# Performance work log

Hardware: AMD Instinct MI355X
Metric: run time of the kernel (lower is better)

The kernel has to match this reference:

```python
import jax, jax.numpy as jnp
import numpy as np

H = W = 56; C = 128; WS = 7; SS = 3; NH = 4; P = 5
HD = C // NH
NWH = H // WS; NWW = W // WS; NW = NWH * NWW
NTOK = WS * WS          # 49 spatial tokens per window
N = NTOK + P            # 54 tokens per window incl. prompts
MLP_H = 4 * C


def _rel_pos_index():
    coords = np.stack(np.meshgrid(np.arange(WS), np.arange(WS), indexing='ij'))  # (2,ws,ws)
    cf = coords.reshape(2, -1)
    rel = (cf[:, :, None] - cf[:, None, :]).transpose(1, 2, 0).copy()
    rel[:, :, 0] += WS - 1
    rel[:, :, 1] += WS - 1
    rel[:, :, 0] *= 2 * WS - 1
    return rel.sum(-1)  # (49,49) int


def _attn_mask():
    # standard shifted-window mask, -100 on cross-region pairs, padded with 0 for prompts
    img = np.zeros((H, W))
    cnt = 0
    for hs in (slice(0, -WS), slice(-WS, -SS), slice(-SS, None)):
        for ws_ in (slice(0, -WS), slice(-WS, -SS), slice(-SS, None)):
            img[hs, ws_] = cnt
            cnt += 1
    mw = img.reshape(NWH, WS, NWW, WS).transpose(0, 2, 1, 3).reshape(-1, NTOK)
    am = mw[:, None, :] - mw[:, :, None]
    am = np.where(am != 0, -100.0, 0.0).astype(np.float32)  # (nW,49,49)
    return np.pad(am, ((0, 0), (P, 0), (P, 0)))  # (nW,54,54)


def layer_norm(x, g, b):
    mu = x.mean(-1, keepdims=True)
    var = ((x - mu) ** 2).mean(-1, keepdims=True)
    return (x - mu) * jax.lax.rsqrt(var + 1e-5) * g + b


def setup_inputs() -> dict:
    key = jax.random.key(0)
    ks = jax.random.split(key, 8)
    s = 0.02
    return {
        'x': jax.random.normal(ks[0], (64, P + H * W, C), jnp.float32),
        'norm1_g': jnp.ones((C,), jnp.float32),
        'norm1_b': jnp.zeros((C,), jnp.float32),
        'qkv_w': jax.random.normal(ks[1], (C, 3 * C), jnp.float32) * s,
        'qkv_b': jnp.zeros((3 * C,), jnp.float32),
        'proj_w': jax.random.normal(ks[2], (C, C), jnp.float32) * s,
        'proj_b': jnp.zeros((C,), jnp.float32),
        'rpb_table': jax.random.normal(ks[3], ((2 * WS - 1) ** 2, NH), jnp.float32) * s,
        'norm2_g': jnp.ones((C,), jnp.float32),
        'norm2_b': jnp.zeros((C,), jnp.float32),
        'fc1_w': jax.random.normal(ks[4], (C, MLP_H), jnp.float32) * s,
        'fc1_b': jnp.zeros((MLP_H,), jnp.float32),
        'fc2_w': jax.random.normal(ks[5], (MLP_H, C), jnp.float32) * s,
        'fc2_b': jnp.zeros((C,), jnp.float32),
    }


def reference(x, norm1_g, norm1_b, qkv_w, qkv_b, proj_w, proj_b, rpb_table,
              norm2_g, norm2_b, fc1_w, fc1_b, fc2_w, fc2_b):
    B = x.shape[0]
    shortcut = x
    xn = layer_norm(x, norm1_g, norm1_b)
    prompt = xn[:, :P]                                  # (B,P,C)
    xs = xn[:, P:].reshape(B, H, W, C)
    xs = jnp.roll(xs, (-SS, -SS), axis=(1, 2))          # cyclic shift
    # window partition -> (B*nW, 49, C), batch-major
    xw = xs.reshape(B, NWH, WS, NWW, WS, C).transpose(0, 1, 3, 2, 4, 5).reshape(B * NW, NTOK, C)
    # prompt expansion: VPT uses expand(nW,...).reshape(-1) => window-major ordering (faithful)
    pe = jnp.broadcast_to(prompt[None], (NW, B, P, C)).reshape(NW * B, P, C)
    xw = jnp.concatenate([pe, xw], axis=1)              # (B*nW, N, C)
    # windowed multi-head attention
    qkv = (xw @ qkv_w + qkv_b).reshape(-1, N, 3, NH, HD).transpose(2, 0, 3, 1, 4)
    q, k, v = qkv[0] * (HD ** -0.5), qkv[1], qkv[2]     # (B*nW, NH, N, HD)
    attn = jnp.einsum('whnd,whmd->whnm', q, k)
    rpb = rpb_table[jnp.asarray(_rel_pos_index().reshape(-1))].reshape(NTOK, NTOK, NH).transpose(2, 0, 1)
    rpb = jnp.pad(rpb, ((0, 0), (P, 0), (P, 0)))        # zeros for prompt rows/cols
    attn = attn + rpb[None]
    mask = jnp.asarray(_attn_mask())                    # (nW,N,N)
    attn = attn.reshape(B, NW, NH, N, N) + mask[None, :, None]
    attn = jax.nn.softmax(attn.reshape(-1, NH, N, N), axis=-1)
    out = jnp.einsum('whnm,whmd->whnd', attn, v).transpose(0, 2, 1, 3).reshape(-1, N, C)
    out = out @ proj_w + proj_b
    # split prompts back out, average across windows (view(-1,B,...) => window-major, faithful)
    prompt_out = out[:, :P].reshape(NW, B, P, C).mean(0)
    spat = out[:, P:].reshape(B, NWH, NWW, WS, WS, C).transpose(0, 1, 3, 2, 4, 5).reshape(B, H, W, C)
    spat = jnp.roll(spat, (SS, SS), axis=(1, 2)).reshape(B, H * W, C)
    xo = jnp.concatenate([prompt_out, spat], axis=1)
    x = shortcut + xo
    h = layer_norm(x, norm2_g, norm2_b)
    h = jax.nn.gelu(h @ fc1_w + fc1_b, approximate=False)
    h = h @ fc2_w + fc2_b
    return x + h
```

## Files before the change

### kernel.cpp

```cpp
#include <hip/hip_runtime.h>
#include <hip/hip_bf16.h>
#include <math.h>


typedef __attribute__((ext_vector_type(8))) short bf16x8;
typedef __attribute__((ext_vector_type(4))) float f32x4;
typedef __attribute__((ext_vector_type(4))) unsigned short u16x4;

__device__ __forceinline__ float bf2f(unsigned short u) {
  union { unsigned int i; float f; } v; v.i = ((unsigned)u) << 16; return v.f;
}
__device__ __forceinline__ unsigned short f2b(float f) {
  __hip_bfloat16 b = __float2bfloat16(f);
  return *reinterpret_cast<unsigned short*>(&b);
}

__global__ __launch_bounds__(256) void convert_wt(const float* __restrict__ w,
    __hip_bfloat16* __restrict__ wt, int K, int N)
{
  int idx = blockIdx.x * 256 + threadIdx.x;
  if (idx >= N * K) return;
  int n = idx / K, k = idx % K;
  wt[idx] = __float2bfloat16(w[(size_t)k * N + n]);
}

__global__ __launch_bounds__(256) void bias_gen(const float* __restrict__ rpb,
    __hip_bfloat16* __restrict__ tab)
{
  int w = blockIdx.x >> 2, h = blockIdx.x & 3;
  int wh = w >> 3, ww = w & 7;
  #pragma unroll
  for (int e = 0; e < 16; ++e) {
    int fi = e * 256 + threadIdx.x;
    int q = fi >> 6, k = fi & 63;
    float v;
    if (k >= 54) {
      v = -INFINITY;
    } else {
      v = 0.f;
      if (q >= 5 && q < 54 && k >= 5) {
        int tq = q - 5, tk = k - 5;
        int aq = tq / 7, bq_ = tq % 7, ak = tk / 7, bk = tk % 7;
        int dh = aq - ak + 6, dw = bq_ - bk + 6;
        v = rpb[(dh * 13 + dw) * 4 + h];
        int rq = wh * 7 + aq, cq = ww * 7 + bq_;
        int rk = wh * 7 + ak, ck = ww * 7 + bk;
        int zq = (rq < 49 ? 0 : (rq < 53 ? 1 : 2)) * 3 + (cq < 49 ? 0 : (cq < 53 ? 1 : 2));
        int zk = (rk < 49 ? 0 : (rk < 53 ? 1 : 2)) * 3 + (ck < 49 ? 0 : (ck < 53 ? 1 : 2));
        if (zq != zk) v += -100.f;
      }
      v *= 1.44269504088896f;
    }
    tab[((size_t)blockIdx.x << 12) + fi] = __float2bfloat16(v);
  }
}

__global__ __launch_bounds__(256, 3) void phase1_fused(
    const float* __restrict__ x,
    const float* __restrict__ n1g, const float* __restrict__ n1b,
    const __hip_bfloat16* __restrict__ w_qkv, const float* __restrict__ qkv_b,
    const __hip_bfloat16* __restrict__ w_prj, const float* __restrict__ proj_b,
    const __hip_bfloat16* __restrict__ bias_tab,
    float* __restrict__ out, float* __restrict__ pbuf)
{
  __shared__ short lds[24576];
  short* xn = lds;
  const int tid = threadIdx.x;
  const int wv = tid >> 6, lane = tid & 63;
  const int c = lane & 15, g = lane >> 4;
  const int gi = blockIdx.x;
  const int w = gi & 63;
  short* Lh = lds + wv * 6144;

  float v0a[14], v1a[14];
  #pragma unroll
  for (int rr = 0; rr < 14; ++rr) {
    int row = wv + rr * 4;
    int rowc = (row < 54) ? row : 0;
    int src;
    if (rowc < 5) {
      src = (gi & 63) * 3141 + rowc;
    } else {
      int b = gi >> 6, t = rowc - 5;
      int hp = (w >> 3) * 7 + t / 7 + 3; if (hp >= 56) hp -= 56;
      int wp = (w & 7) * 7 + t % 7 + 3;  if (wp >= 56) wp -= 56;
      src = b * 3141 + 5 + hp * 56 + wp;
    }
    const float* xr = x + (size_t)src * 128;
    v0a[rr] = xr[lane];
    v1a[rr] = xr[lane + 64];
  }
  #pragma unroll
  for (int rr = 0; rr < 14; ++rr) {
    int row = wv + rr * 4;
    if (row < 54) {
      float v0 = v0a[rr], v1 = v1a[rr];
      float s = v0 + v1, s2 = v0 * v0 + v1 * v1;
      #pragma unroll
      for (int off = 32; off > 0; off >>= 1) {
        s  += __shfl_xor(s,  off);
        s2 += __shfl_xor(s2, off);
      }
      float mu = s * (1.f / 128.f);
      float var = s2 * (1.f / 128.f) - mu * mu;
      float rs = rsqrtf(var + 1e-5f);
      float y0 = (v0 - mu) * rs * n1g[lane]      + n1b[lane];
      float y1 = (v1 - mu) * rs * n1g[lane + 64] + n1b[lane + 64];
      int f = (row & 15) >> 1;
      int ca = lane, cb = lane + 64;
      xn[row * 128 + (((ca >> 3) ^ f) << 3) + (ca & 7)] = (short)f2b(y0);
      xn[row * 128 + (((cb >> 3) ^ f) << 3) + (cb & 7)] = (short)f2b(y1);
    }
  }
  for (int idx = tid; idx < 1280; idx += 256) xn[54 * 128 + idx] = 0;
  __syncthreads();

  bf16x8 af[4][4];
  #pragma unroll
  for (int ks = 0; ks < 4; ++ks)
    #pragma unroll
    for (int mi = 0; mi < 4; ++mi) {
      int row = mi * 16 + c;
      af[ks][mi] = *(const bf16x8*)(xn + row * 128 +
                    (((ks * 4 + g) ^ ((row & 15) >> 1)) << 3));
    }
  const unsigned short* bt = (const unsigned short*)bias_tab + ((size_t)(w * 4 + wv) << 12);
  u16x4 bb[4][4];
  #pragma unroll
  for (int ni = 0; ni < 4; ++ni)
    #pragma unroll
    for (int mi = 0; mi < 4; ++mi)
      bb[ni][mi] = *(const u16x4*)(bt + (ni * 16 + c) * 64 + mi * 16 + g * 4);
  __syncthreads();

  {
    #pragma unroll
    for (int t = 0; t < 6; ++t) {
      int m = t >> 1;
      int chb = (t & 1) * 16;
      int n0 = m * 128 + wv * 32 + chb;
      bf16x8 bfr[4];
      #pragma unroll
      for (int ks = 0; ks < 4; ++ks)
        bfr[ks] = *(const bf16x8*)(w_qkv + (size_t)(n0 + c) * 128 + ks * 32 + g * 8);
      f32x4 acct[4] = {};
      __builtin_amdgcn_s_setprio(1);
      #pragma unroll
      for (int ks = 0; ks < 4; ++ks)
        #pragma unroll
        for (int mi = 0; mi < 4; ++mi)
          acct[mi] = __builtin_amdgcn_mfma_f32_16x16x32_bf16(
              bfr[ks], af[ks][mi], acct[mi], 0, 0, 0);
      __builtin_amdgcn_s_setprio(0);
      f32x4 bq4 = *(const f32x4*)(qkv_b + n0 + g * 4);
      int cpart = (chb >> 3) + (g >> 1);
      #pragma unroll
      for (int mi = 0; mi < 4; ++mi) {
        int tok = mi * 16 + c;
        int swz = (m == 2) ? ((tok >> 3) & 3) : ((tok >> 1) & 3);
        u16x4 pw;
        #pragma unroll
        for (int r = 0; r < 4; ++r) pw[r] = f2b(acct[mi][r] + bq4[r]);
        *(u16x4*)(Lh + m * 2048 + tok * 32 + ((cpart ^ swz) << 3) + (g & 1) * 4) = pw;
      }
    }
  }

  {
    const int h = wv;
    bf16x8 kf[4], bq[4];
    #pragma unroll
    for (int mi = 0; mi < 4; ++mi) {
      int tok = mi * 16 + c;
      kf[mi] = *(const bf16x8*)(Lh + 2048 + tok * 32 + ((g ^ ((tok >> 1) & 3)) << 3));
    }
    #pragma unroll
    for (int ni = 0; ni < 4; ++ni) {
      int q = ni * 16 + c;
      bq[ni] = *(const bf16x8*)(Lh + q * 32 + ((g ^ ((q >> 1) & 3)) << 3));
    }
    f32x4 acc[4][4] = {};
    __builtin_amdgcn_s_setprio(1);
    #pragma unroll
    for (int mi = 0; mi < 4; ++mi)
      #pragma unroll
      for (int ni = 0; ni < 4; ++ni)
        acc[mi][ni] = __builtin_amdgcn_mfma_f32_16x16x32_bf16(kf[mi], bq[ni], acc[mi][ni], 0, 0, 0);
    __builtin_amdgcn_s_setprio(0);

    const float SC = 0.17677669529663689f * 1.44269504088896f;
    #pragma unroll
    for (int ni = 0; ni < 4; ++ni)
      #pragma unroll
      for (int mi = 0; mi < 4; ++mi)
        #pragma unroll
        for (int r = 0; r < 4; ++r)
          acc[mi][ni][r] = acc[mi][ni][r] * SC + bf2f(bb[ni][mi][r]);

    #pragma unroll
    for (int ni = 0; ni < 4; ++ni) {
      float m2 = -3.0e38f;
      #pragma unroll
      for (int mi = 0; mi < 4; ++mi)
        #pragma unroll
        for (int r = 0; r < 4; ++r)
          m2 = fmaxf(m2, acc[mi][ni][r]);
      m2 = fmaxf(m2, __shfl_xor(m2, 16, 64));
      m2 = fmaxf(m2, __shfl_xor(m2, 32, 64));
      float sm = 0.f;
      #pragma unroll
      for (int mi = 0; mi < 4; ++mi)
        #pragma unroll
        for (int r = 0; r < 4; ++r) {
          float p = exp2f(acc[mi][ni][r] - m2);
          acc[mi][ni][r] = p;
          sm += p;
        }
      sm += __shfl_xor(sm, 16, 64);
      sm += __shfl_xor(sm, 32, 64);
      float inv = 1.0f / sm;
      int q = ni * 16 + c;
      #pragma unroll
      for (int mi = 0; mi < 4; ++mi) {
        u16x4 pw;
        #pragma unroll
        for (int r = 0; r < 4; ++r) pw[r] = f2b(acc[mi][ni][r] * inv);
        int chp = (mi * 2 + (g >> 1)) ^ (q & 7);
        *(u16x4*)(Lh + q * 64 + chp * 8 + (g & 1) * 4) = pw;
      }
    }

    f32x4 acc2[2][4] = {};
    #pragma unroll
    for (int ks = 0; ks < 2; ++ks) {
      bf16x8 pa[4];
      #pragma unroll
      for (int qi = 0; qi < 4; ++qi) {
        int q = qi * 16 + c;
        int chk = (ks * 4 + g) ^ (q & 7);
        pa[qi] = *(const bf16x8*)(Lh + q * 64 + chk * 8);
      }
      bf16x8 vb[2];
      #pragma unroll
      for (int di = 0; di < 2; ++di) {
        #pragma unroll
        for (int j = 0; j < 8; ++j) {
          int k = ks * 32 + g * 8 + j;
          int chv = ((di * 2 + (c >> 3)) ^ g);
          vb[di][j] = Lh[4096 + k * 32 + chv * 8 + (c & 7)];
        }
      }
      __builtin_amdgcn_s_setprio(1);
      #pragma unroll
      for (int qi = 0; qi < 4; ++qi)
        #pragma unroll
        for (int di = 0; di < 2; ++di)
          acc2[di][qi] = __builtin_amdgcn_mfma_f32_16x16x32_bf16(vb[di], pa[qi], acc2[di][qi], 0, 0, 0);
      __builtin_amdgcn_s_setprio(0);
    }

    __syncthreads();
    #pragma unroll
    for (int di = 0; di < 2; ++di) {
      int chunk = h * 4 + di * 2 + (g >> 1);
      #pragma unroll
      for (int qi = 0; qi < 4; ++qi) {
        int tok = qi * 16 + c;
        u16x4 pw;
        #pragma unroll
        for (int r = 0; r < 4; ++r) pw[r] = f2b(acc2[di][qi][r]);
        *(u16x4*)(xn + tok * 128 + ((chunk ^ (c >> 1)) << 3) + (g & 1) * 4) = pw;
      }
    }
  }
  __syncthreads();

  {
    f32x4 accp[4][2] = {};
    #pragma unroll
    for (int ks = 0; ks < 4; ++ks) {
      bf16x8 afp[4];
      #pragma unroll
      for (int mi = 0; mi < 4; ++mi) {
        int row = mi * 16 + c;
        afp[mi] = *(const bf16x8*)(xn + row * 128 +
                   (((ks * 4 + g) ^ ((row & 15) >> 1)) << 3));
      }
      bf16x8 wfp[2];
      #pragma unroll
      for (int ni = 0; ni < 2; ++ni)
        wfp[ni] = *(const bf16x8*)(w_prj +
            (size_t)(wv * 32 + ni * 16 + c) * 128 + ks * 32 + g * 8);
      #pragma unroll
      for (int mi = 0; mi < 4; ++mi)
        #pragma unroll
        for (int ni = 0; ni < 2; ++ni)
          accp[mi][ni] = __builtin_amdgcn_mfma_f32_16x16x32_bf16(
              afp[mi], wfp[ni], accp[mi][ni], 0, 0, 0);
    }
    float pb[2];
    pb[0] = proj_b[wv * 32 + c];
    pb[1] = proj_b[wv * 32 + 16 + c];
    #pragma unroll
    for (int mi = 0; mi < 4; ++mi) {
      #pragma unroll
      for (int r = 0; r < 4; ++r) {
        int tok = mi * 16 + g * 4 + r;
        if (tok < 54) {
          if (tok < 5) {
            #pragma unroll
            for (int ni = 0; ni < 2; ++ni) {
              int gcol = wv * 32 + ni * 16 + c;
              pbuf[((size_t)gi * 5 + tok) * 128 + gcol] = accp[mi][ni][r] + pb[ni];
            }
          } else {
            int b = gi >> 6, tt = tok - 5;
            int rr2 = (w >> 3) * 7 + tt / 7 + 3; if (rr2 >= 56) rr2 -= 56;
            int cc = (w & 7) * 7 + tt % 7 + 3;   if (cc >= 56) cc -= 56;
            size_t ob = ((size_t)b * 3141 + 5 + rr2 * 56 + cc) * 128;
            #pragma unroll
            for (int ni = 0; ni < 2; ++ni) {
              int gcol = wv * 32 + ni * 16 + c;
              out[ob + gcol] = x[ob + gcol] + accp[mi][ni][r] + pb[ni];
            }
          }
        }
      }
    }
  }
}

__global__ __launch_bounds__(128) void prompt_reduce(const float* __restrict__ x,
    const float* __restrict__ pbuf, float* __restrict__ out)
{
  int bp = blockIdx.x;
  int b = bp / 5, p = bp % 5;
  int c = threadIdx.x;
  float s = 0.f;
  for (int w = 0; w < 64; ++w)
    s += pbuf[((size_t)(w * 64 + b) * 5 + p) * 128 + c];
  size_t oidx = ((size_t)b * 3141 + p) * 128 + c;
  out[oidx] = x[oidx] + s * (1.f / 64.f);
}

__device__ __forceinline__ void mlp_fc1(const short* __restrict__ xn,
    short* __restrict__ dst, const __hip_bfloat16* __restrict__ w1t,
    const float* __restrict__ b1, int s, int wv, int c, int g)
{
  bf16x8 wf[4][2];
  #pragma unroll
  for (int ks = 0; ks < 4; ++ks)
    #pragma unroll
    for (int ni = 0; ni < 2; ++ni)
      wf[ks][ni] = *(const bf16x8*)(w1t +
          (size_t)(s * 128 + wv * 32 + ni * 16 + c) * 128 + ks * 32 + g * 8);
  f32x4 acc1[2][4] = {};
  #pragma unroll
  for (int ks = 0; ks < 4; ++ks) {
    bf16x8 af[4];
    #pragma unroll
    for (int mi = 0; mi < 4; ++mi) {
      int row = mi * 16 + c;
      af[mi] = *(const bf16x8*)(xn + row * 128 +
                                (((ks * 4 + g) ^ ((row & 15) >> 1)) << 3));
    }
    #pragma unroll
    for (int mi = 0; mi < 4; ++mi)
      #pragma unroll
      for (int ni = 0; ni < 2; ++ni)
        acc1[ni][mi] = __builtin_amdgcn_mfma_f32_16x16x32_bf16(
            wf[ks][ni], af[mi], acc1[ni][mi], 0, 0, 0);
  }
  #pragma unroll
  for (int ni = 0; ni < 2; ++ni) {
    f32x4 b1v = *(const f32x4*)(b1 + s * 128 + wv * 32 + ni * 16 + g * 4);
    int chunk = wv * 4 + ni * 2 + (g >> 1);
    #pragma unroll
    for (int mi = 0; mi < 4; ++mi) {
      int tok = mi * 16 + c;
      u16x4 pw;
      #pragma unroll
      for (int r = 0; r < 4; ++r) {
        float t = acc1[ni][mi][r] + b1v[r];
        float u = t * (0.7978845608028654f + 0.0356774081f * t * t);
        float e = exp2f(-2.8853900817779268f * u);
        t = t * __builtin_amdgcn_rcpf(1.0f + e);
        pw[r] = f2b(t);
      }
      *(u16x4*)(dst + tok * 128 + ((chunk ^ (c >> 1)) << 3) + (g & 1) * 4) = pw;
    }
  }
}

__device__ __forceinline__ void mlp_fc2(const short* __restrict__ hsrc,
    const __hip_bfloat16* __restrict__ w2t, f32x4 (&acc2)[4][2],
    int s, int wv, int c, int g)
{
  bf16x8 wf[4][2];
  #pragma unroll
  for (int ks = 0; ks < 4; ++ks)
    #pragma unroll
    for (int ni = 0; ni < 2; ++ni)
      wf[ks][ni] = *(const bf16x8*)(w2t +
          (size_t)(wv * 32 + ni * 16 + c) * 512 + s * 128 + ks * 32 + g * 8);
  #pragma unroll
  for (int ks = 0; ks < 4; ++ks) {
    bf16x8 af[4];
    #pragma unroll
    for (int mi = 0; mi < 4; ++mi) {
      int row = mi * 16 + c;
      af[mi] = *(const bf16x8*)(hsrc + row * 128 +
                                (((ks * 4 + g) ^ ((row & 15) >> 1)) << 3));
    }
    #pragma unroll
    for (int mi = 0; mi < 4; ++mi)
      #pragma unroll
      for (int ni = 0; ni < 2; ++ni)
        acc2[mi][ni] = __builtin_amdgcn_mfma_f32_16x16x32_bf16(
            af[mi], wf[ks][ni], acc2[mi][ni], 0, 0, 0);
  }
}

__global__ __launch_bounds__(256, 3) void mlp_fused(
    const float* __restrict__ xin,
    const float* __restrict__ gamma, const float* __restrict__ beta,
    const __hip_bfloat16* __restrict__ w1t, const float* __restrict__ b1,
    const __hip_bfloat16* __restrict__ w2t, const float* __restrict__ b2,
    float* __restrict__ outp)
{
  __shared__ short xn[8192];
  __shared__ short hb[2][8192];
  const int tid = threadIdx.x;
  const int wv = tid >> 6, lane = tid & 63;
  const int c = lane & 15, g = lane >> 4;
  const int r0 = blockIdx.x * 64;

  float v0a[16], v1a[16];
  #pragma unroll
  for (int rr = 0; rr < 16; ++rr) {
    int row = wv * 16 + rr;
    const float* xr = xin + (size_t)(r0 + row) * 128;
    v0a[rr] = xr[lane];
    v1a[rr] = xr[lane + 64];
  }
  #pragma unroll
  for (int rr = 0; rr < 16; ++rr) {
    int row = wv * 16 + rr;
    float v0 = v0a[rr], v1 = v1a[rr];
    float s = v0 + v1, s2 = v0 * v0 + v1 * v1;
    #pragma unroll
    for (int off = 32; off > 0; off >>= 1) {
      s  += __shfl_xor(s,  off);
      s2 += __shfl_xor(s2, off);
    }
    float mu = s * (1.f / 128.f);
    float var = s2 * (1.f / 128.f) - mu * mu;
    float rs = rsqrtf(var + 1e-5f);
    float y0 = (v0 - mu) * rs * gamma[lane]      + beta[lane];
    float y1 = (v1 - mu) * rs * gamma[lane + 64] + beta[lane + 64];
    int f = (row & 15) >> 1;
    int ca = lane, cb = lane + 64;
    xn[row * 128 + (((ca >> 3) ^ f) << 3) + (ca & 7)] = (short)f2b(y0);
    xn[row * 128 + (((cb >> 3) ^ f) << 3) + (cb & 7)] = (short)f2b(y1);
  }
  __syncthreads();

  mlp_fc1(xn, hb[0], w1t, b1, 0, wv, c, g);
  __syncthreads();

  f32x4 acc2[4][2] = {};
  #pragma unroll
  for (int s = 0; s < 4; ++s) {
    if (s < 3) mlp_fc1(xn, hb[(s + 1) & 1], w1t, b1, s + 1, wv, c, g);
    mlp_fc2(hb[s & 1], w2t, acc2, s, wv, c, g);
    if (s < 3) __syncthreads();
  }

  #pragma unroll
  for (int mi = 0; mi < 4; ++mi) {
    #pragma unroll
    for (int r = 0; r < 4; ++r) {
      int row = r0 + mi * 16 + g * 4 + r;
      #pragma unroll
      for (int ni = 0; ni < 2; ++ni) {
        int col = wv * 32 + ni * 16 + c;
        size_t o = (size_t)row * 128 + col;
        outp[o] = acc2[mi][ni][r] + b2[col] + xin[o];
      }
    }
  }
}

extern "C" void kernel_launch(void* const* d_in, const int* in_sizes, int n_in,
                              void* d_out, int out_size, void* d_ws, size_t ws_size,
                              hipStream_t stream) {
  const float* x      = (const float*)d_in[0];
  const float* n1g    = (const float*)d_in[1];
  const float* n1b    = (const float*)d_in[2];
  const float* qkv_w  = (const float*)d_in[3];
  const float* qkv_b  = (const float*)d_in[4];
  const float* proj_w = (const float*)d_in[5];
  const float* proj_b = (const float*)d_in[6];
  const float* rpb    = (const float*)d_in[7];
  const float* n2g    = (const float*)d_in[8];
  const float* n2b    = (const float*)d_in[9];
  const float* fc1w   = (const float*)d_in[10];
  const float* fc1b   = (const float*)d_in[11];
  const float* fc2w   = (const float*)d_in[12];
  const float* fc2b   = (const float*)d_in[13];
  float* out = (float*)d_out;
  char* ws = (char*)d_ws;

  __hip_bfloat16* wbuf = (__hip_bfloat16*)ws;
  __hip_bfloat16* w_qkv = wbuf;
  __hip_bfloat16* w_prj = wbuf + 49152;
  __hip_bfloat16* w_fc1 = wbuf + 65536;
  __hip_bfloat16* w_fc2 = wbuf + 131072;
  __hip_bfloat16* bias_tab = (__hip_bfloat16*)(ws + 393216);
  float* pbuf = (float*)(ws + 2490368);

  hipLaunchKernelGGL(convert_wt, dim3(192), dim3(256), 0, stream, qkv_w, w_qkv, 128, 384);
  hipLaunchKernelGGL(convert_wt, dim3(64),  dim3(256), 0, stream, proj_w, w_prj, 128, 128);
  hipLaunchKernelGGL(convert_wt, dim3(256), dim3(256), 0, stream, fc1w,  w_fc1, 128, 512);
  hipLaunchKernelGGL(convert_wt, dim3(256), dim3(256), 0, stream, fc2w,  w_fc2, 512, 128);
  hipLaunchKernelGGL(bias_gen, dim3(256), dim3(256), 0, stream, rpb, bias_tab);

  hipLaunchKernelGGL(phase1_fused, dim3(4096), dim3(256), 0, stream,
                     x, n1g, n1b, w_qkv, qkv_b, w_prj, proj_b, bias_tab, out, pbuf);
  hipLaunchKernelGGL(prompt_reduce, dim3(320), dim3(128), 0, stream, x, pbuf, out);

  hipLaunchKernelGGL(mlp_fused, dim3(3141), dim3(256), 0, stream,
                     out, n2g, n2b, w_fc1, fc1b, w_fc2, fc2b, out);
  (void)in_sizes; (void)n_in; (void)out_size; (void)ws_size;
}
```

Baseline: 323.8 us.

## Keep Q/K and softmax probabilities in registers, shrink LDS for higher occupancy

Q and K projections are computed with a permuted weight-row order so their MFMA accumulators can be packed directly into B/A fragments for the QK^T MFMA, skipping the LDS round trip. Softmax probabilities are likewise packed in registers as operands for the PV MFMA, and only V is staged in LDS (per-wave 2048 shorts). This cuts LDS from 48KB to 32KB, lets launch bounds rise to 4 blocks per CU, and removes one barrier. The cost is higher register pressure under the tighter bound, which may cause spills; the rel-pos bias load is also moved later.

```diff
diff --git a/kernel.cpp b/kernel.cpp
--- a/kernel.cpp
+++ b/kernel.cpp
@@ -14,6 +14,10 @@
   __hip_bfloat16 b = __float2bfloat16(f);
   return *reinterpret_cast<unsigned short*>(&b);
 }
+__device__ __forceinline__ unsigned pkbf(float lo, float hi) {
+  return ((unsigned)f2b(hi) << 16) | (unsigned)f2b(lo);
+}
+union Pk8 { bf16x8 v; unsigned w[4]; };
 
 __global__ __launch_bounds__(256) void convert_wt(const float* __restrict__ w,
     __hip_bfloat16* __restrict__ wt, int K, int N)
@@ -55,7 +59,7 @@
   }
 }
 
-__global__ __launch_bounds__(256, 3) void phase1_fused(
+__global__ __launch_bounds__(256, 4) void phase1_fused(
     const float* __restrict__ x,
     const float* __restrict__ n1g, const float* __restrict__ n1b,
     const __hip_bfloat16* __restrict__ w_qkv, const float* __restrict__ qkv_b,
@@ -63,15 +67,17 @@
     const __hip_bfloat16* __restrict__ bias_tab,
     float* __restrict__ out, float* __restrict__ pbuf)
 {
-  __shared__ short lds[24576];
+  __shared__ short lds[16384];
   short* xn = lds;
   const int tid = threadIdx.x;
   const int wv = tid >> 6, lane = tid & 63;
   const int c = lane & 15, g = lane >> 4;
   const int gi = blockIdx.x;
   const int w = gi & 63;
-  short* Lh = lds + wv * 6144;
-
+  short* Vb = lds + 8192 + wv * 2048;
+
+  float g0 = n1g[lane], g1 = n1g[lane + 64];
+  float b0 = n1b[lane], b1 = n1b[lane + 64];
   float v0a[14], v1a[14];
   #pragma unroll
   for (int rr = 0; rr < 14; ++rr) {
@@ -104,8 +110,8 @@
       float mu = s * (1.f / 128.f);
       float var = s2 * (1.f / 128.f) - mu * mu;
       float rs = rsqrtf(var + 1e-5f);
-      float y0 = (v0 - mu) * rs * n1g[lane]      + n1b[lane];
-      float y1 = (v1 - mu) * rs * n1g[lane + 64] + n1b[lane + 64];
+      float y0 = (v0 - mu) * rs * g0 + b0;
+      float y1 = (v1 - mu) * rs * g1 + b1;
       int f = (row & 15) >> 1;
       int ca = lane, cb = lane + 64;
       xn[row * 128 + (((ca >> 3) ^ f) << 3) + (ca & 7)] = (short)f2b(y0);
@@ -124,25 +130,19 @@
       af[ks][mi] = *(const bf16x8*)(xn + row * 128 +
                     (((ks * 4 + g) ^ ((row & 15) >> 1)) << 3));
     }
-  const unsigned short* bt = (const unsigned short*)bias_tab + ((size_t)(w * 4 + wv) << 12);
-  u16x4 bb[4][4];
-  #pragma unroll
-  for (int ni = 0; ni < 4; ++ni)
-    #pragma unroll
-    for (int mi = 0; mi < 4; ++mi)
-      bb[ni][mi] = *(const u16x4*)(bt + (ni * 16 + c) * 64 + mi * 16 + g * 4);
-  __syncthreads();
-
-  {
-    #pragma unroll
-    for (int t = 0; t < 6; ++t) {
-      int m = t >> 1;
-      int chb = (t & 1) * 16;
-      int n0 = m * 128 + wv * 32 + chb;
+
+  bf16x8 bq[4], kf[4];
+  #pragma unroll
+  for (int qk = 0; qk < 2; ++qk) {
+    f32x4 a0[4] = {}, a1[4] = {};
+    #pragma unroll
+    for (int tt = 0; tt < 2; ++tt) {
       bf16x8 bfr[4];
       #pragma unroll
       for (int ks = 0; ks < 4; ++ks)
-        bfr[ks] = *(const bf16x8*)(w_qkv + (size_t)(n0 + c) * 128 + ks * 32 + g * 8);
+        bfr[ks] = *(const bf16x8*)(w_qkv +
+            (size_t)(qk * 128 + wv * 32 + (c >> 2) * 8 + tt * 4 + (c & 3)) * 128 +
+            ks * 32 + g * 8);
       f32x4 acct[4] = {};
       __builtin_amdgcn_s_setprio(1);
       #pragma unroll
@@ -152,125 +152,156 @@
           acct[mi] = __builtin_amdgcn_mfma_f32_16x16x32_bf16(
               bfr[ks], af[ks][mi], acct[mi], 0, 0, 0);
       __builtin_amdgcn_s_setprio(0);
-      f32x4 bq4 = *(const f32x4*)(qkv_b + n0 + g * 4);
-      int cpart = (chb >> 3) + (g >> 1);
-      #pragma unroll
-      for (int mi = 0; mi < 4; ++mi) {
-        int tok = mi * 16 + c;
-        int swz = (m == 2) ? ((tok >> 3) & 3) : ((tok >> 1) & 3);
-        u16x4 pw;
-        #pragma unroll
-        for (int r = 0; r < 4; ++r) pw[r] = f2b(acct[mi][r] + bq4[r]);
-        *(u16x4*)(Lh + m * 2048 + tok * 32 + ((cpart ^ swz) << 3) + (g & 1) * 4) = pw;
-      }
-    }
-  }
-
-  {
-    const int h = wv;
-    bf16x8 kf[4], bq[4];
-    #pragma unroll
-    for (int mi = 0; mi < 4; ++mi) {
-      int tok = mi * 16 + c;
-      kf[mi] = *(const bf16x8*)(Lh + 2048 + tok * 32 + ((g ^ ((tok >> 1) & 3)) << 3));
-    }
-    #pragma unroll
-    for (int ni = 0; ni < 4; ++ni) {
-      int q = ni * 16 + c;
-      bq[ni] = *(const bf16x8*)(Lh + q * 32 + ((g ^ ((q >> 1) & 3)) << 3));
-    }
-    f32x4 acc[4][4] = {};
-    __builtin_amdgcn_s_setprio(1);
-    #pragma unroll
-    for (int mi = 0; mi < 4; ++mi)
-      #pragma unroll
-      for (int ni = 0; ni < 4; ++ni)
-        acc[mi][ni] = __builtin_amdgcn_mfma_f32_16x16x32_bf16(kf[mi], bq[ni], acc[mi][ni], 0, 0, 0);
-    __builtin_amdgcn_s_setprio(0);
-
-    const float SC = 0.17677669529663689f * 1.44269504088896f;
-    #pragma unroll
-    for (int ni = 0; ni < 4; ++ni)
-      #pragma unroll
-      for (int mi = 0; mi < 4; ++mi)
-        #pragma unroll
-        for (int r = 0; r < 4; ++r)
-          acc[mi][ni][r] = acc[mi][ni][r] * SC + bf2f(bb[ni][mi][r]);
-
-    #pragma unroll
-    for (int ni = 0; ni < 4; ++ni) {
-      float m2 = -3.0e38f;
-      #pragma unroll
-      for (int mi = 0; mi < 4; ++mi)
-        #pragma unroll
-        for (int r = 0; r < 4; ++r)
-          m2 = fmaxf(m2, acc[mi][ni][r]);
-      m2 = fmaxf(m2, __shfl_xor(m2, 16, 64));
-      m2 = fmaxf(m2, __shfl_xor(m2, 32, 64));
-      float sm = 0.f;
+      f32x4 bv = *(const f32x4*)(qkv_b + qk * 128 + wv * 32 + g * 8 + tt * 4);
       #pragma unroll
       for (int mi = 0; mi < 4; ++mi)
         #pragma unroll
         for (int r = 0; r < 4; ++r) {
-          float p = exp2f(acc[mi][ni][r] - m2);
-          acc[mi][ni][r] = p;
-          sm += p;
+          float t = acct[mi][r] + bv[r];
+          if (tt) a1[mi][r] = t; else a0[mi][r] = t;
         }
-      sm += __shfl_xor(sm, 16, 64);
-      sm += __shfl_xor(sm, 32, 64);
-      float inv = 1.0f / sm;
-      int q = ni * 16 + c;
-      #pragma unroll
-      for (int mi = 0; mi < 4; ++mi) {
-        u16x4 pw;
-        #pragma unroll
-        for (int r = 0; r < 4; ++r) pw[r] = f2b(acc[mi][ni][r] * inv);
-        int chp = (mi * 2 + (g >> 1)) ^ (q & 7);
-        *(u16x4*)(Lh + q * 64 + chp * 8 + (g & 1) * 4) = pw;
-      }
-    }
-
-    f32x4 acc2[2][4] = {};
-    #pragma unroll
-    for (int ks = 0; ks < 2; ++ks) {
-      bf16x8 pa[4];
-      #pragma unroll
-      for (int qi = 0; qi < 4; ++qi) {
-        int q = qi * 16 + c;
-        int chk = (ks * 4 + g) ^ (q & 7);
-        pa[qi] = *(const bf16x8*)(Lh + q * 64 + chk * 8);
-      }
-      bf16x8 vb[2];
-      #pragma unroll
-      for (int di = 0; di < 2; ++di) {
-        #pragma unroll
-        for (int j = 0; j < 8; ++j) {
-          int k = ks * 32 + g * 8 + j;
-          int chv = ((di * 2 + (c >> 3)) ^ g);
-          vb[di][j] = Lh[4096 + k * 32 + chv * 8 + (c & 7)];
-        }
-      }
-      __builtin_amdgcn_s_setprio(1);
-      #pragma unroll
-      for (int qi = 0; qi < 4; ++qi)
-        #pragma unroll
-        for (int di = 0; di < 2; ++di)
-          acc2[di][qi] = __builtin_amdgcn_mfma_f32_16x16x32_bf16(vb[di], pa[qi], acc2[di][qi], 0, 0, 0);
-      __builtin_amdgcn_s_setprio(0);
-    }
-
-    __syncthreads();
+    }
+    #pragma unroll
+    for (int mi = 0; mi < 4; ++mi) {
+      Pk8 u;
+      u.w[0] = pkbf(a0[mi][0], a0[mi][1]);
+      u.w[1] = pkbf(a0[mi][2], a0[mi][3]);
+      u.w[2] = pkbf(a1[mi][0], a1[mi][1]);
+      u.w[3] = pkbf(a1[mi][2], a1[mi][3]);
+      if (qk) kf[mi] = u.v; else bq[mi] = u.v;
+    }
+  }
+
+  #pragma unroll
+  for (int tt = 0; tt < 2; ++tt) {
+    int chb = tt * 16;
+    int n0 = 256 + wv * 32 + chb;
+    bf16x8 bfr[4];
+    #pragma unroll
+    for (int ks = 0; ks < 4; ++ks)
+      bfr[ks] = *(const bf16x8*)(w_qkv + (size_t)(n0 + c) * 128 + ks * 32 + g * 8);
+    f32x4 acct[4] = {};
+    __builtin_amdgcn_s_setprio(1);
+    #pragma unroll
+    for (int ks = 0; ks < 4; ++ks)
+      #pragma unroll
+      for (int mi = 0; mi < 4; ++mi)
+        acct[mi] = __builtin_amdgcn_mfma_f32_16x16x32_bf16(
+            bfr[ks], af[ks][mi], acct[mi], 0, 0, 0);
+    __builtin_amdgcn_s_setprio(0);
+    f32x4 bv = *(const f32x4*)(qkv_b + n0 + g * 4);
+    int cpart = (chb >> 3) + (g >> 1);
+    #pragma unroll
+    for (int mi = 0; mi < 4; ++mi) {
+      int tok = mi * 16 + c;
+      int swz = (tok >> 3) & 3;
+      u16x4 pw;
+      #pragma unroll
+      for (int r = 0; r < 4; ++r) pw[r] = f2b(acct[mi][r] + bv[r]);
+      *(u16x4*)(Vb + tok * 32 + ((cpart ^ swz) << 3) + (g & 1) * 4) = pw;
+    }
+  }
+
+  f32x4 acc[4][4] = {};
+  __builtin_amdgcn_s_setprio(1);
+  #pragma unroll
+  for (int mi = 0; mi < 4; ++mi)
+    #pragma unroll
+    for (int ni = 0; ni < 4; ++ni)
+      acc[mi][ni] = __builtin_amdgcn_mfma_f32_16x16x32_bf16(
+          kf[mi], bq[ni], acc[mi][ni], 0, 0, 0);
+  __builtin_amdgcn_s_setprio(0);
+
+  const unsigned short* bt = (const unsigned short*)bias_tab + ((size_t)(w * 4 + wv) << 12);
+  u16x4 bb[4][4];
+  #pragma unroll
+  for (int ni = 0; ni < 4; ++ni)
+    #pragma unroll
+    for (int mi = 0; mi < 4; ++mi)
+      bb[ni][mi] = *(const u16x4*)(bt + (ni * 16 + c) * 64 + mi * 16 + g * 4);
+
+  const float SC = 0.17677669529663689f * 1.44269504088896f;
+  #pragma unroll
+  for (int ni = 0; ni < 4; ++ni)
+    #pragma unroll
+    for (int mi = 0; mi < 4; ++mi)
+      #pragma unroll
+      for (int r = 0; r < 4; ++r)
+        acc[mi][ni][r] = acc[mi][ni][r] * SC + bf2f(bb[ni][mi][r]);
+
+  #pragma unroll
+  for (int ni = 0; ni < 4; ++ni) {
+    float m2 = -3.0e38f;
+    #pragma unroll
+    for (int mi = 0; mi < 4; ++mi)
+      #pragma unroll
+      for (int r = 0; r < 4; ++r)
+        m2 = fmaxf(m2, acc[mi][ni][r]);
+    m2 = fmaxf(m2, __shfl_xor(m2, 16, 64));
+    m2 = fmaxf(m2, __shfl_xor(m2, 32, 64));
+    float sm = 0.f;
+    #pragma unroll
+    for (int mi = 0; mi < 4; ++mi)
+      #pragma unroll
+      for (int r = 0; r < 4; ++r) {
+        float p = exp2f(acc[mi][ni][r] - m2);
+        acc[mi][ni][r] = p;
+        sm += p;
+      }
+    sm += __shfl_xor(sm, 16, 64);
+    sm += __shfl_xor(sm, 32, 64);
+    float inv = 1.0f / sm;
+    #pragma unroll
+    for (int mi = 0; mi < 4; ++mi)
+      #pragma unroll
+      for (int r = 0; r < 4; ++r)
+        acc[mi][ni][r] *= inv;
+  }
+
+  f32x4 acc2[2][4] = {};
+  #pragma unroll
+  for (int ks = 0; ks < 2; ++ks) {
+    bf16x8 pa[4];
+    #pragma unroll
+    for (int qi = 0; qi < 4; ++qi) {
+      Pk8 u;
+      u.w[0] = pkbf(acc[2 * ks][qi][0],     acc[2 * ks][qi][1]);
+      u.w[1] = pkbf(acc[2 * ks][qi][2],     acc[2 * ks][qi][3]);
+      u.w[2] = pkbf(acc[2 * ks + 1][qi][0], acc[2 * ks + 1][qi][1]);
+      u.w[3] = pkbf(acc[2 * ks + 1][qi][2], acc[2 * ks + 1][qi][3]);
+      pa[qi] = u.v;
+    }
+    bf16x8 vb[2];
     #pragma unroll
     for (int di = 0; di < 2; ++di) {
-      int chunk = h * 4 + di * 2 + (g >> 1);
-      #pragma unroll
-      for (int qi = 0; qi < 4; ++qi) {
-        int tok = qi * 16 + c;
-        u16x4 pw;
-        #pragma unroll
-        for (int r = 0; r < 4; ++r) pw[r] = f2b(acc2[di][qi][r]);
-        *(u16x4*)(xn + tok * 128 + ((chunk ^ (c >> 1)) << 3) + (g & 1) * 4) = pw;
-      }
+      #pragma unroll
+      for (int j = 0; j < 8; ++j) {
+        int ptok = (2 * ks + (j >> 2)) * 16 + g * 4 + (j & 3);
+        int pswz = (2 * (j >> 2) + (g >> 1)) & 3;
+        vb[di][j] = Vb[ptok * 32 + (((di * 2 + (c >> 3)) ^ pswz) << 3) + (c & 7)];
+      }
+    }
+    __builtin_amdgcn_s_setprio(1);
+    #pragma unroll
+    for (int qi = 0; qi < 4; ++qi)
+      #pragma unroll
+      for (int di = 0; di < 2; ++di)
+        acc2[di][qi] = __builtin_amdgcn_mfma_f32_16x16x32_bf16(
+            vb[di], pa[qi], acc2[di][qi], 0, 0, 0);
+    __builtin_amdgcn_s_setprio(0);
+  }
+
+  __syncthreads();
+  #pragma unroll
+  for (int di = 0; di < 2; ++di) {
+    int chunk = wv * 4 + di * 2 + (g >> 1);
+    #pragma unroll
+    for (int qi = 0; qi < 4; ++qi) {
+      int tok = qi * 16 + c;
+      u16x4 pw;
+      #pragma unroll
+      for (int r = 0; r < 4; ++r) pw[r] = f2b(acc2[di][qi][r]);
+      *(u16x4*)(xn + tok * 128 + ((chunk ^ (c >> 1)) << 3) + (g & 1) * 4) = pw;
     }
   }
   __syncthreads();
```

Measured after the change: 397.6 us. 1.23x slower.
